# Kernel tuning notes

Hardware: AMD Instinct MI355X
Metric: run time of the kernel (lower is better)

Reference implementation:

```python
import jax, jax.numpy as jnp
import numpy as np
from jax import lax

K = 3
PAD = 1
STRIDE = 1


def setup_inputs() -> dict:
    key = jax.random.key(0)
    k1, k2, k3 = jax.random.split(key, 3)
    B, Cin, Cout, H, W = 4, 64, 64, 128, 128
    x = jax.random.normal(k1, (B, Cin, H, W), dtype=jnp.float32)
    # offset-generating conv weight: [2*K*K, Cin, K, K]
    w_offset = jax.random.normal(k2, (2 * K * K, Cin, K, K), dtype=jnp.float32) * 0.05
    # deformable conv weight: [Cout, Cin, K, K]
    w_deform = jax.random.normal(k3, (Cout, Cin, K, K), dtype=jnp.float32) * 0.05
    return {"x": x, "w_offset": w_offset, "w_deform": w_deform}


def _bilinear_sample_one(img, ys, xs):
    # img: [C, H, W]; ys, xs: [K2, Ho, Wo] float sampling coords
    H, W = img.shape[1], img.shape[2]
    y0 = jnp.floor(ys)
    x0 = jnp.floor(xs)
    wy = ys - y0  # frac weights, [K2, Ho, Wo]
    wx = xs - x0

    def gather(yi, xi):
        valid = (yi >= 0) & (yi <= H - 1) & (xi >= 0) & (xi <= W - 1)
        yc = jnp.clip(yi, 0, H - 1).astype(jnp.int32)
        xc = jnp.clip(xi, 0, W - 1).astype(jnp.int32)
        # img[:, yc, xc] -> [C, K2, Ho, Wo]; zero outside (torchvision zero-pad)
        return img[:, yc, xc] * valid[None].astype(img.dtype)

    v00 = gather(y0, x0)
    v01 = gather(y0, x0 + 1)
    v10 = gather(y0 + 1, x0)
    v11 = gather(y0 + 1, x0 + 1)
    w00 = ((1 - wy) * (1 - wx))[None]
    w01 = ((1 - wy) * wx)[None]
    w10 = (wy * (1 - wx))[None]
    w11 = (wy * wx)[None]
    return v00 * w00 + v01 * w01 + v10 * w10 + v11 * w11  # [C, K2, Ho, Wo]


def reference(x, w_offset, w_deform):
    B, Cin, H, W = x.shape
    Cout = w_deform.shape[0]
    K2 = K * K
    # 1) plain conv to produce offsets: [B, 2*K2, H, W]
    offset = lax.conv_general_dilated(
        x, w_offset, window_strides=(STRIDE, STRIDE),
        padding=((PAD, PAD), (PAD, PAD)),
        dimension_numbers=("NCHW", "OIHW", "NCHW"))
    Ho, Wo = offset.shape[2], offset.shape[3]
    # torchvision ordering: channel 2*k = dy, 2*k+1 = dx, taps row-major
    off = offset.reshape(B, K2, 2, Ho, Wo)
    dy, dx = off[:, :, 0], off[:, :, 1]  # [B, K2, Ho, Wo]
    # 2) base sampling grid per kernel tap
    kk = jnp.arange(K2)
    ki = (kk // K).astype(jnp.float32)  # tap row
    kj = (kk % K).astype(jnp.float32)   # tap col
    base_y = (jnp.arange(Ho, dtype=jnp.float32) * STRIDE - PAD)[None, :] + ki[:, None]  # [K2, Ho]
    base_x = (jnp.arange(Wo, dtype=jnp.float32) * STRIDE - PAD)[None, :] + kj[:, None]  # [K2, Wo]
    ys = base_y[None, :, :, None] + dy  # [B, K2, Ho, Wo]
    xs = base_x[None, :, None, :] + dx
    # 3) deformable bilinear gather: [B, Cin, K2, Ho, Wo]
    sampled = jax.vmap(_bilinear_sample_one)(x, ys, xs)
    # 4) weighted accumulation (the conv contraction)
    out = jnp.einsum("ock,bckhw->bohw", w_deform.reshape(Cout, Cin, K2), sampled)
    return out
```

## Files before the change

kernel.cpp:

```cpp
#include <hip/hip_runtime.h>


#define BATCH 4
#define CIN   64
#define COUT  64
#define HH    128
#define WW    128
#define HWPIX (HH*WW)

typedef __attribute__((ext_vector_type(8))) short short8;
typedef __attribute__((ext_vector_type(4))) float floatx4;

__device__ __forceinline__ unsigned short f2bf(float f) {
  unsigned int u = __float_as_uint(f);
  unsigned int r = u + 0x7fffu + ((u >> 16) & 1u);
  return (unsigned short)(r >> 16);
}
__device__ __forceinline__ float bf2f(unsigned short h) { return __uint_as_float(((unsigned int)h) << 16); }
__device__ __forceinline__ float lo16f(unsigned int u) { return __uint_as_float(u << 16); }
__device__ __forceinline__ float hi16f(unsigned int u) { return __uint_as_float(u & 0xffff0000u); }

__device__ __forceinline__ unsigned int bilin2(unsigned int u00, unsigned int u01,
                                               unsigned int u10, unsigned int u11,
                                               float w00, float w01, float w10, float w11) {
  float lo = w00 * lo16f(u00) + w01 * lo16f(u01) + w10 * lo16f(u10) + w11 * lo16f(u11);
  float hi = w00 * hi16f(u00) + w01 * hi16f(u01) + w10 * hi16f(u10) + w11 * hi16f(u11);
  return (unsigned int)f2bf(lo) | ((unsigned int)f2bf(hi) << 16);
}

__global__ __launch_bounds__(256) void transpose_x_kernel(const float* __restrict__ x,
                                                          unsigned short* __restrict__ xThi,
                                                          unsigned short* __restrict__ xTlo) {
  __shared__ float tile[32][33];
  int b = blockIdx.z, p0 = blockIdx.x * 32, c0 = blockIdx.y * 32;
  int tx = threadIdx.x, ty = threadIdx.y;
  const float* xb = x + (size_t)b * CIN * HWPIX;
  size_t boff = (size_t)b * HWPIX * CIN;
#pragma unroll
  for (int i = 0; i < 4; i++)
    tile[ty + i * 8][tx] = xb[(size_t)(c0 + ty + i * 8) * HWPIX + p0 + tx];
  __syncthreads();
  int wid = ty * 32 + tx;
#pragma unroll
  for (int i = 0; i < 2; i++) {
    int t = wid + i * 256;
    int row = t >> 4;
    int cp = t & 15;
    float v0 = tile[cp * 2][row], v1 = tile[cp * 2 + 1][row];
    unsigned short h0 = f2bf(v0), h1 = f2bf(v1);
    unsigned short l0 = f2bf(v0 - bf2f(h0)), l1 = f2bf(v1 - bf2f(h1));
    size_t o = boff + (size_t)(p0 + row) * CIN + c0 + cp * 2;
    *(ushort2*)&xThi[o] = make_ushort2(h0, h1);
    *(ushort2*)&xTlo[o] = make_ushort2(l0, l1);
  }
}

__global__ __launch_bounds__(256) void prep_weights_kernel(const float* __restrict__ wo,
                                                           const float* __restrict__ wd,
                                                           unsigned short* __restrict__ wdA,
                                                           unsigned short* __restrict__ woAhi,
                                                           unsigned short* __restrict__ woAlo) {
  int t = blockIdx.x * 256 + threadIdx.x;
  if (t < 36864) {
    int j = t & 7, lane = (t >> 3) & 63, ct = (t >> 9) & 3, kc = (t >> 11) & 1, kk = t >> 12;
    int cout = ct * 16 + (lane & 15);
    int cin  = kc * 32 + (lane >> 4) * 8 + j;
    wdA[t] = f2bf(wd[(size_t)(cout * CIN + cin) * 9 + kk]);
  }
  int t2 = t - 36864;
  if (t2 >= 0 && t2 < 18432) {
    int j = t2 & 7, lane = (t2 >> 3) & 63, ct = (t2 >> 9) & 1, kc = (t2 >> 10) & 1, kk = t2 >> 11;
    int cout = ct * 16 + (lane & 15);
    int cin  = kc * 32 + (lane >> 4) * 8 + j;
    float v = (cout < 18) ? wo[(size_t)(cout * CIN + cin) * 9 + kk] : 0.f;
    unsigned short h = f2bf(v);
    woAhi[t2] = h;
    woAlo[t2] = f2bf(v - bf2f(h));
  }
}

__global__ __launch_bounds__(256) void offset_mfma_kernel(const unsigned short* __restrict__ xThi,
                                                          const unsigned short* __restrict__ xTlo,
                                                          const unsigned short* __restrict__ woAhi,
                                                          const unsigned short* __restrict__ woAlo,
                                                          float* __restrict__ offs) {
  __shared__ unsigned short sBhi[4096];
  __shared__ unsigned short sBlo[4096];
  int tid = threadIdx.x;
  int hw = blockIdx.x;
  int bid = (hw & 7) * 128 + (hw >> 3);
  int b = bid >> 8, r = bid & 255, y = r >> 1, x0 = (r & 1) << 6;

  int p1 = tid >> 2, si = tid & 3;
  int lane = tid & 63, w = tid >> 6;

  const unsigned short* xhib = xThi + (size_t)b * HWPIX * CIN;
  const unsigned short* xlob = xTlo + (size_t)b * HWPIX * CIN;

  int wq = p1 >> 4, iq = p1 & 15;
  int kcd = si >> 1, qb = si & 1;
  int dst0 = (((wq * 2 + kcd) * 64) + qb * 32 + iq) * 8;
  int dst1 = dst0 + 128;

  floatx4 acc[2];
  acc[0] = (floatx4){0.f, 0.f, 0.f, 0.f};
  acc[1] = (floatx4){0.f, 0.f, 0.f, 0.f};

  int xp = x0 + p1;

#pragma unroll 1
  for (int kk = 0; kk < 9; kk++) {
    int ys = y - 1 + kk / 3;
    int xs = xp - 1 + kk % 3;
    bool valid = (ys >= 0) && (ys < HH) && (xs >= 0) && (xs < WW);
    uint4 h0 = {0, 0, 0, 0}, h1 = {0, 0, 0, 0}, l0 = {0, 0, 0, 0}, l1 = {0, 0, 0, 0};
    if (valid) {
      const unsigned short* ph = xhib + (size_t)(ys * WW + xs) * CIN + si * 16;
      const unsigned short* pl = xlob + (size_t)(ys * WW + xs) * CIN + si * 16;
      h0 = *(const uint4*)ph; h1 = *(const uint4*)(ph + 8);
      l0 = *(const uint4*)pl; l1 = *(const uint4*)(pl + 8);
    }
    *(uint4*)&sBhi[dst0] = h0; *(uint4*)&sBhi[dst1] = h1;
    *(uint4*)&sBlo[dst0] = l0; *(uint4*)&sBlo[dst1] = l1;
    __syncthreads();
    short8 bh0 = *(const short8*)&sBhi[(w * 2 + 0) * 512 + lane * 8];
    short8 bh1 = *(const short8*)&sBhi[(w * 2 + 1) * 512 + lane * 8];
    short8 bl0 = *(const short8*)&sBlo[(w * 2 + 0) * 512 + lane * 8];
    short8 bl1 = *(const short8*)&sBlo[(w * 2 + 1) * 512 + lane * 8];
    const short8* Ah = (const short8*)(woAhi + (size_t)kk * 2048);
    const short8* Al = (const short8*)(woAlo + (size_t)kk * 2048);
#pragma unroll
    for (int ct = 0; ct < 2; ct++) {
      short8 ah0 = Ah[ct * 64 + lane], ah1 = Ah[128 + ct * 64 + lane];
      short8 al0 = Al[ct * 64 + lane], al1 = Al[128 + ct * 64 + lane];
      acc[ct] = __builtin_amdgcn_mfma_f32_16x16x32_bf16(ah0, bh0, acc[ct], 0, 0, 0);
      acc[ct] = __builtin_amdgcn_mfma_f32_16x16x32_bf16(ah0, bl0, acc[ct], 0, 0, 0);
      acc[ct] = __builtin_amdgcn_mfma_f32_16x16x32_bf16(al0, bh0, acc[ct], 0, 0, 0);
      acc[ct] = __builtin_amdgcn_mfma_f32_16x16x32_bf16(ah1, bh1, acc[ct], 0, 0, 0);
      acc[ct] = __builtin_amdgcn_mfma_f32_16x16x32_bf16(ah1, bl1, acc[ct], 0, 0, 0);
      acc[ct] = __builtin_amdgcn_mfma_f32_16x16x32_bf16(al1, bh1, acc[ct], 0, 0, 0);
    }
    __syncthreads();
  }

  int px = x0 + w * 16 + (lane & 15);
  int rowb = (lane >> 4) * 4;
  float* ob = offs + (size_t)b * 18 * HWPIX + y * WW + px;
#pragma unroll
  for (int ct = 0; ct < 2; ct++)
#pragma unroll
    for (int rr = 0; rr < 4; rr++) {
      int row = ct * 16 + rowb + rr;
      if (row < 18) ob[(size_t)row * HWPIX] = acc[ct][rr];
    }
}

__global__ __launch_bounds__(256) void deform_gemm_kernel(const unsigned short* __restrict__ xT,
                                                          const float* __restrict__ offs,
                                                          const unsigned short* __restrict__ wdA,
                                                          float* __restrict__ out) {
  __shared__ unsigned short sampB[4096];
  int tid = threadIdx.x;
  int hw = blockIdx.x;
  int bid = (hw & 7) * 128 + (hw >> 3);
  int b = bid >> 8, r = bid & 255, y = r >> 1, x0 = (r & 1) << 6;

  int p1 = tid >> 2, si = tid & 3;
  int lane = tid & 63, w = tid >> 6;

  const unsigned short* xTb = xT + (size_t)b * HWPIX * CIN;
  const float* ob = offs + (size_t)b * 18 * HWPIX + y * WW + (x0 + p1);

  int wq = p1 >> 4, iq = p1 & 15;
  int kcd = si >> 1, qb = si & 1;
  int dst0 = (((wq * 2 + kcd) * 64) + qb * 32 + iq) * 8;
  int dst1 = dst0 + 128;

  floatx4 acc[4];
#pragma unroll
  for (int ct = 0; ct < 4; ct++) acc[ct] = (floatx4){0.f, 0.f, 0.f, 0.f};

  int xp = x0 + p1;

#pragma unroll 1
  for (int kk = 0; kk < 9; kk++) {
    {
      float dy = ob[(size_t)(2 * kk) * HWPIX];
      float dx = ob[(size_t)(2 * kk + 1) * HWPIX];
      float ys = (float)(y - 1 + kk / 3) + dy;
      float xs = (float)(xp - 1 + kk % 3) + dx;
      float y0f = floorf(ys), x0f = floorf(xs);
      float wy = ys - y0f, wx = xs - x0f;
      int iy0 = (int)y0f, ix0 = (int)x0f;
      int iy1 = iy0 + 1, ix1 = ix0 + 1;
      float w00 = (1.f - wy) * (1.f - wx), w01 = (1.f - wy) * wx;
      float w10 = wy * (1.f - wx), w11 = wy * wx;
      bool vy0 = (iy0 >= 0) && (iy0 < HH), vy1 = (iy1 >= 0) && (iy1 < HH);
      bool vx0 = (ix0 >= 0) && (ix0 < WW), vx1 = (ix1 >= 0) && (ix1 < WW);
      if (!(vy0 && vx0)) w00 = 0.f;
      if (!(vy0 && vx1)) w01 = 0.f;
      if (!(vy1 && vx0)) w10 = 0.f;
      if (!(vy1 && vx1)) w11 = 0.f;
      int cy0 = min(max(iy0, 0), HH - 1), cy1 = min(max(iy1, 0), HH - 1);
      int cx0 = min(max(ix0, 0), WW - 1), cx1 = min(max(ix1, 0), WW - 1);
      const unsigned short* q00 = xTb + (size_t)(cy0 * WW + cx0) * CIN + si * 16;
      const unsigned short* q01 = xTb + (size_t)(cy0 * WW + cx1) * CIN + si * 16;
      const unsigned short* q10 = xTb + (size_t)(cy1 * WW + cx0) * CIN + si * 16;
      const unsigned short* q11 = xTb + (size_t)(cy1 * WW + cx1) * CIN + si * 16;
      uint4 a00 = *(const uint4*)q00, a01 = *(const uint4*)q01;
      uint4 a10 = *(const uint4*)q10, a11 = *(const uint4*)q11;
      uint4 b00 = *(const uint4*)(q00 + 8), b01 = *(const uint4*)(q01 + 8);
      uint4 b10 = *(const uint4*)(q10 + 8), b11 = *(const uint4*)(q11 + 8);
      uint4 o0, o1;
      o0.x = bilin2(a00.x, a01.x, a10.x, a11.x, w00, w01, w10, w11);
      o0.y = bilin2(a00.y, a01.y, a10.y, a11.y, w00, w01, w10, w11);
      o0.z = bilin2(a00.z, a01.z, a10.z, a11.z, w00, w01, w10, w11);
      o0.w = bilin2(a00.w, a01.w, a10.w, a11.w, w00, w01, w10, w11);
      o1.x = bilin2(b00.x, b01.x, b10.x, b11.x, w00, w01, w10, w11);
      o1.y = bilin2(b00.y, b01.y, b10.y, b11.y, w00, w01, w10, w11);
      o1.z = bilin2(b00.z, b01.z, b10.z, b11.z, w00, w01, w10, w11);
      o1.w = bilin2(b00.w, b01.w, b10.w, b11.w, w00, w01, w10, w11);
      *(uint4*)&sampB[dst0] = o0;
      *(uint4*)&sampB[dst1] = o1;
    }
    __syncthreads();
    {
      short8 bv0 = *(const short8*)&sampB[(w * 2 + 0) * 512 + lane * 8];
      short8 bv1 = *(const short8*)&sampB[(w * 2 + 1) * 512 + lane * 8];
      const short8* Ap = (const short8*)(wdA + (size_t)kk * 4096);
#pragma unroll
      for (int ct = 0; ct < 4; ct++) {
        short8 a0 = Ap[ct * 64 + lane];
        short8 a1 = Ap[256 + ct * 64 + lane];
        acc[ct] = __builtin_amdgcn_mfma_f32_16x16x32_bf16(a0, bv0, acc[ct], 0, 0, 0);
        acc[ct] = __builtin_amdgcn_mfma_f32_16x16x32_bf16(a1, bv1, acc[ct], 0, 0, 0);
      }
    }
    __syncthreads();
  }

  int px = x0 + w * 16 + (lane & 15);
  int rowb = (lane >> 4) * 4;
  float* outb = out + (size_t)b * COUT * HWPIX + y * WW + px;
#pragma unroll
  for (int ct = 0; ct < 4; ct++)
#pragma unroll
    for (int rr = 0; rr < 4; rr++)
      outb[(size_t)(ct * 16 + rowb + rr) * HWPIX] = acc[ct][rr];
}

extern "C" void kernel_launch(void* const* d_in, const int* in_sizes, int n_in,
                              void* d_out, int out_size, void* d_ws, size_t ws_size,
                              hipStream_t stream) {
  const float* x  = (const float*)d_in[0];
  const float* wo = (const float*)d_in[1];
  const float* wd = (const float*)d_in[2];
  float* out = (float*)d_out;

  char* wsb = (char*)d_ws;
  unsigned short* xThi  = (unsigned short*)wsb;
  unsigned short* xTlo  = (unsigned short*)(wsb + 8388608);
  float* offs           = (float*)(wsb + 16777216);
  unsigned short* wdA   = (unsigned short*)(wsb + 16777216 + 4718592);
  unsigned short* woAhi = (unsigned short*)(wsb + 21495808 + 73728);
  unsigned short* woAlo = (unsigned short*)(wsb + 21569536 + 36864);

  transpose_x_kernel<<<dim3(HWPIX / 32, CIN / 32, BATCH), dim3(32, 8, 1), 0, stream>>>(x, xThi, xTlo);
  prep_weights_kernel<<<dim3(216), dim3(256), 0, stream>>>(wo, wd, wdA, woAhi, woAlo);
  offset_mfma_kernel<<<dim3(BATCH * HWPIX / 64), dim3(256), 0, stream>>>(xThi, xTlo, woAhi, woAlo, offs);
  deform_gemm_kernel<<<dim3(BATCH * HWPIX / 64), dim3(256), 0, stream>>>(xThi, offs, wdA, out);
}
```

Baseline: 122.3 us.

## Fuse offset conv into deformable GEMM kernel and merge prep kernels

Merges the x transpose and weight-prep kernels into one launch, and fuses the offset-conv MFMA kernel with the deformable sampling GEMM. Offsets now stay in shared memory per 64-pixel block instead of going through a global buffer, and the sampled tile reuses the sBhi shared buffer. This removes two kernel launches and the global write and read of the offset tensor. The cost is higher per-block shared memory and register pressure in the fused kernel, which may lower occupancy.

After: 114.6 us. 1.07x faster.

```diff
diff --git a/kernel.cpp b/kernel.cpp
--- a/kernel.cpp
+++ b/kernel.cpp
@@ -28,64 +28,70 @@
   return (unsigned int)f2bf(lo) | ((unsigned int)f2bf(hi) << 16);
 }
 
-__global__ __launch_bounds__(256) void transpose_x_kernel(const float* __restrict__ x,
-                                                          unsigned short* __restrict__ xThi,
-                                                          unsigned short* __restrict__ xTlo) {
-  __shared__ float tile[32][33];
-  int b = blockIdx.z, p0 = blockIdx.x * 32, c0 = blockIdx.y * 32;
-  int tx = threadIdx.x, ty = threadIdx.y;
-  const float* xb = x + (size_t)b * CIN * HWPIX;
-  size_t boff = (size_t)b * HWPIX * CIN;
-#pragma unroll
-  for (int i = 0; i < 4; i++)
-    tile[ty + i * 8][tx] = xb[(size_t)(c0 + ty + i * 8) * HWPIX + p0 + tx];
-  __syncthreads();
-  int wid = ty * 32 + tx;
-#pragma unroll
-  for (int i = 0; i < 2; i++) {
-    int t = wid + i * 256;
-    int row = t >> 4;
-    int cp = t & 15;
-    float v0 = tile[cp * 2][row], v1 = tile[cp * 2 + 1][row];
-    unsigned short h0 = f2bf(v0), h1 = f2bf(v1);
-    unsigned short l0 = f2bf(v0 - bf2f(h0)), l1 = f2bf(v1 - bf2f(h1));
-    size_t o = boff + (size_t)(p0 + row) * CIN + c0 + cp * 2;
-    *(ushort2*)&xThi[o] = make_ushort2(h0, h1);
-    *(ushort2*)&xTlo[o] = make_ushort2(l0, l1);
-  }
-}
-
-__global__ __launch_bounds__(256) void prep_weights_kernel(const float* __restrict__ wo,
-                                                           const float* __restrict__ wd,
-                                                           unsigned short* __restrict__ wdA,
-                                                           unsigned short* __restrict__ woAhi,
-                                                           unsigned short* __restrict__ woAlo) {
-  int t = blockIdx.x * 256 + threadIdx.x;
-  if (t < 36864) {
-    int j = t & 7, lane = (t >> 3) & 63, ct = (t >> 9) & 3, kc = (t >> 11) & 1, kk = t >> 12;
-    int cout = ct * 16 + (lane & 15);
-    int cin  = kc * 32 + (lane >> 4) * 8 + j;
-    wdA[t] = f2bf(wd[(size_t)(cout * CIN + cin) * 9 + kk]);
-  }
-  int t2 = t - 36864;
-  if (t2 >= 0 && t2 < 18432) {
-    int j = t2 & 7, lane = (t2 >> 3) & 63, ct = (t2 >> 9) & 1, kc = (t2 >> 10) & 1, kk = t2 >> 11;
-    int cout = ct * 16 + (lane & 15);
-    int cin  = kc * 32 + (lane >> 4) * 8 + j;
-    float v = (cout < 18) ? wo[(size_t)(cout * CIN + cin) * 9 + kk] : 0.f;
-    unsigned short h = f2bf(v);
-    woAhi[t2] = h;
-    woAlo[t2] = f2bf(v - bf2f(h));
-  }
-}
-
-__global__ __launch_bounds__(256) void offset_mfma_kernel(const unsigned short* __restrict__ xThi,
-                                                          const unsigned short* __restrict__ xTlo,
-                                                          const unsigned short* __restrict__ woAhi,
-                                                          const unsigned short* __restrict__ woAlo,
-                                                          float* __restrict__ offs) {
+__global__ __launch_bounds__(256) void pre_kernel(const float* __restrict__ x,
+                                                  const float* __restrict__ wo,
+                                                  const float* __restrict__ wd,
+                                                  unsigned short* __restrict__ xThi,
+                                                  unsigned short* __restrict__ xTlo,
+                                                  unsigned short* __restrict__ wdA,
+                                                  unsigned short* __restrict__ woAhi,
+                                                  unsigned short* __restrict__ woAlo) {
+  int tid = threadIdx.x;
+  if (blockIdx.x < 4096) {
+    __shared__ float tile[32][33];
+    int t = blockIdx.x;
+    int b = t >> 10, rem = t & 1023;
+    int c0 = (rem >> 9) * 32, p0 = (rem & 511) * 32;
+    int tx = tid & 31, ty = tid >> 5;
+    const float* xb = x + (size_t)b * CIN * HWPIX;
+    size_t boff = (size_t)b * HWPIX * CIN;
+#pragma unroll
+    for (int i = 0; i < 4; i++)
+      tile[ty + i * 8][tx] = xb[(size_t)(c0 + ty + i * 8) * HWPIX + p0 + tx];
+    __syncthreads();
+#pragma unroll
+    for (int i = 0; i < 2; i++) {
+      int tt = tid + i * 256;
+      int row = tt >> 4;
+      int cp = tt & 15;
+      float v0 = tile[cp * 2][row], v1 = tile[cp * 2 + 1][row];
+      unsigned short h0 = f2bf(v0), h1 = f2bf(v1);
+      unsigned short l0 = f2bf(v0 - bf2f(h0)), l1 = f2bf(v1 - bf2f(h1));
+      size_t o = boff + (size_t)(p0 + row) * CIN + c0 + cp * 2;
+      *(ushort2*)&xThi[o] = make_ushort2(h0, h1);
+      *(ushort2*)&xTlo[o] = make_ushort2(l0, l1);
+    }
+  } else {
+    int t = (blockIdx.x - 4096) * 256 + tid;
+    if (t < 36864) {
+      int j = t & 7, lane = (t >> 3) & 63, ct = (t >> 9) & 3, kc = (t >> 11) & 1, kk = t >> 12;
+      int cout = ct * 16 + (lane & 15);
+      int cin  = kc * 32 + (lane >> 4) * 8 + j;
+      wdA[t] = f2bf(wd[(size_t)(cout * CIN + cin) * 9 + kk]);
+    }
+    int t2 = t - 36864;
+    if (t2 >= 0 && t2 < 18432) {
+      int j = t2 & 7, lane = (t2 >> 3) & 63, ct = (t2 >> 9) & 1, kc = (t2 >> 10) & 1, kk = t2 >> 11;
+      int cout = ct * 16 + (lane & 15);
+      int cin  = kc * 32 + (lane >> 4) * 8 + j;
+      float v = (cout < 18) ? wo[(size_t)(cout * CIN + cin) * 9 + kk] : 0.f;
+      unsigned short h = f2bf(v);
+      woAhi[t2] = h;
+      woAlo[t2] = f2bf(v - bf2f(h));
+    }
+  }
+}
+
+__global__ __launch_bounds__(256) void fused_dcn_kernel(const unsigned short* __restrict__ xThi,
+                                                        const unsigned short* __restrict__ xTlo,
+                                                        const unsigned short* __restrict__ woAhi,
+                                                        const unsigned short* __restrict__ woAlo,
+                                                        const unsigned short* __restrict__ wdA,
+                                                        float* __restrict__ out) {
   __shared__ unsigned short sBhi[4096];
   __shared__ unsigned short sBlo[4096];
+  __shared__ float offL[18 * 64];
+
   int tid = threadIdx.x;
   int hw = blockIdx.x;
   int bid = (hw & 7) * 128 + (hw >> 3);
@@ -101,12 +107,11 @@
   int kcd = si >> 1, qb = si & 1;
   int dst0 = (((wq * 2 + kcd) * 64) + qb * 32 + iq) * 8;
   int dst1 = dst0 + 128;
-
-  floatx4 acc[2];
-  acc[0] = (floatx4){0.f, 0.f, 0.f, 0.f};
-  acc[1] = (floatx4){0.f, 0.f, 0.f, 0.f};
-
   int xp = x0 + p1;
+
+  floatx4 oacc[2];
+  oacc[0] = (floatx4){0.f, 0.f, 0.f, 0.f};
+  oacc[1] = (floatx4){0.f, 0.f, 0.f, 0.f};
 
 #pragma unroll 1
   for (int kk = 0; kk < 9; kk++) {
@@ -133,60 +138,38 @@
     for (int ct = 0; ct < 2; ct++) {
       short8 ah0 = Ah[ct * 64 + lane], ah1 = Ah[128 + ct * 64 + lane];
       short8 al0 = Al[ct * 64 + lane], al1 = Al[128 + ct * 64 + lane];
-      acc[ct] = __builtin_amdgcn_mfma_f32_16x16x32_bf16(ah0, bh0, acc[ct], 0, 0, 0);
-      acc[ct] = __builtin_amdgcn_mfma_f32_16x16x32_bf16(ah0, bl0, acc[ct], 0, 0, 0);
-      acc[ct] = __builtin_amdgcn_mfma_f32_16x16x32_bf16(al0, bh0, acc[ct], 0, 0, 0);
-      acc[ct] = __builtin_amdgcn_mfma_f32_16x16x32_bf16(ah1, bh1, acc[ct], 0, 0, 0);
-      acc[ct] = __builtin_amdgcn_mfma_f32_16x16x32_bf16(ah1, bl1, acc[ct], 0, 0, 0);
-      acc[ct] = __builtin_amdgcn_mfma_f32_16x16x32_bf16(al1, bh1, acc[ct], 0, 0, 0);
-    }
-    __syncthreads();
-  }
-
-  int px = x0 + w * 16 + (lane & 15);
-  int rowb = (lane >> 4) * 4;
-  float* ob = offs + (size_t)b * 18 * HWPIX + y * WW + px;
-#pragma unroll
-  for (int ct = 0; ct < 2; ct++)
-#pragma unroll
-    for (int rr = 0; rr < 4; rr++) {
-      int row = ct * 16 + rowb + rr;
-      if (row < 18) ob[(size_t)row * HWPIX] = acc[ct][rr];
-    }
-}
-
-__global__ __launch_bounds__(256) void deform_gemm_kernel(const unsigned short* __restrict__ xT,
-                                                          const float* __restrict__ offs,
-                                                          const unsigned short* __restrict__ wdA,
-                                                          float* __restrict__ out) {
-  __shared__ unsigned short sampB[4096];
-  int tid = threadIdx.x;
-  int hw = blockIdx.x;
-  int bid = (hw & 7) * 128 + (hw >> 3);
-  int b = bid >> 8, r = bid & 255, y = r >> 1, x0 = (r & 1) << 6;
-
-  int p1 = tid >> 2, si = tid & 3;
-  int lane = tid & 63, w = tid >> 6;
-
-  const unsigned short* xTb = xT + (size_t)b * HWPIX * CIN;
-  const float* ob = offs + (size_t)b * 18 * HWPIX + y * WW + (x0 + p1);
-
-  int wq = p1 >> 4, iq = p1 & 15;
-  int kcd = si >> 1, qb = si & 1;
-  int dst0 = (((wq * 2 + kcd) * 64) + qb * 32 + iq) * 8;
-  int dst1 = dst0 + 128;
+      oacc[ct] = __builtin_amdgcn_mfma_f32_16x16x32_bf16(ah0, bh0, oacc[ct], 0, 0, 0);
+      oacc[ct] = __builtin_amdgcn_mfma_f32_16x16x32_bf16(ah0, bl0, oacc[ct], 0, 0, 0);
+      oacc[ct] = __builtin_amdgcn_mfma_f32_16x16x32_bf16(al0, bh0, oacc[ct], 0, 0, 0);
+      oacc[ct] = __builtin_amdgcn_mfma_f32_16x16x32_bf16(ah1, bh1, oacc[ct], 0, 0, 0);
+      oacc[ct] = __builtin_amdgcn_mfma_f32_16x16x32_bf16(ah1, bl1, oacc[ct], 0, 0, 0);
+      oacc[ct] = __builtin_amdgcn_mfma_f32_16x16x32_bf16(al1, bh1, oacc[ct], 0, 0, 0);
+    }
+    __syncthreads();
+  }
+
+  {
+    int pxl = w * 16 + (lane & 15);
+    int rowb = (lane >> 4) * 4;
+#pragma unroll
+    for (int ct = 0; ct < 2; ct++)
+#pragma unroll
+      for (int rr = 0; rr < 4; rr++) {
+        int row = ct * 16 + rowb + rr;
+        if (row < 18) offL[row * 64 + pxl] = oacc[ct][rr];
+      }
+  }
+  __syncthreads();
 
   floatx4 acc[4];
 #pragma unroll
   for (int ct = 0; ct < 4; ct++) acc[ct] = (floatx4){0.f, 0.f, 0.f, 0.f};
-
-  int xp = x0 + p1;
 
 #pragma unroll 1
   for (int kk = 0; kk < 9; kk++) {
     {
-      float dy = ob[(size_t)(2 * kk) * HWPIX];
-      float dx = ob[(size_t)(2 * kk + 1) * HWPIX];
+      float dy = offL[(2 * kk) * 64 + p1];
+      float dx = offL[(2 * kk + 1) * 64 + p1];
       float ys = (float)(y - 1 + kk / 3) + dy;
       float xs = (float)(xp - 1 + kk % 3) + dx;
       float y0f = floorf(ys), x0f = floorf(xs);
@@ -203,10 +186,10 @@
       if (!(vy1 && vx1)) w11 = 0.f;
       int cy0 = min(max(iy0, 0), HH - 1), cy1 = min(max(iy1, 0), HH - 1);
       int cx0 = min(max(ix0, 0), WW - 1), cx1 = min(max(ix1, 0), WW - 1);
-      const unsigned short* q00 = xTb + (size_t)(cy0 * WW + cx0) * CIN + si * 16;
-      const unsigned short* q01 = xTb + (size_t)(cy0 * WW + cx1) * CIN + si * 16;
-      const unsigned short* q10 = xTb + (size_t)(cy1 * WW + cx0) * CIN + si * 16;
-      const unsigned short* q11 = xTb + (size_t)(cy1 * WW + cx1) * CIN + si * 16;
+      const unsigned short* q00 = xhib + (size_t)(cy0 * WW + cx0) * CIN + si * 16;
+      const unsigned short* q01 = xhib + (size_t)(cy0 * WW + cx1) * CIN + si * 16;
+      const unsigned short* q10 = xhib + (size_t)(cy1 * WW + cx0) * CIN + si * 16;
+      const unsigned short* q11 = xhib + (size_t)(cy1 * WW + cx1) * CIN + si * 16;
       uint4 a00 = *(const uint4*)q00, a01 = *(const uint4*)q01;
       uint4 a10 = *(const uint4*)q10, a11 = *(const uint4*)q11;
       uint4 b00 = *(const uint4*)(q00 + 8), b01 = *(const uint4*)(q01 + 8);
@@ -220,13 +203,13 @@
       o1.y = bilin2(b00.y, b01.y, b10.y, b11.y, w00, w01, w10, w11);
       o1.z = bilin2(b00.z, b01.z, b10.z, b11.z, w00, w01, w10, w11);
       o1.w = bilin2(b00.w, b01.w, b10.w, b11.w, w00, w01, w10, w11);
-      *(uint4*)&sampB[dst0] = o0;
-      *(uint4*)&sampB[dst1] = o1;
+      *(uint4*)&sBhi[dst0] = o0;
+      *(uint4*)&sBhi[dst1] = o1;
     }
     __syncthreads();
     {
-      short8 bv0 = *(const short8*)&sampB[(w * 2 + 0) * 512 + lane * 8];
-      short8 bv1 = *(const short8*)&sampB[(w * 2 + 1) * 512 + lane * 8];
+      short8 bv0 = *(const short8*)&sBhi[(w * 2 + 0) * 512 + lane * 8];
+      short8 bv1 = *(const short8*)&sBhi[(w * 2 + 1) * 512 + lane * 8];
       const short8* Ap = (const short8*)(wdA + (size_t)kk * 4096);
 #pragma unroll
       for (int ct = 0; ct < 4; ct++) {
@@ -260,13 +243,10 @@
   char* wsb = (char*)d_ws;
   unsigned short* xThi  = (unsigned short*)wsb;
   unsigned short* xTlo  = (unsigned short*)(wsb + 8388608);
-  float* offs           = (float*)(wsb + 16777216);
-  unsigned short* wdA   = (unsigned short*)(wsb + 16777216 + 4718592);
-  unsigned short* woAhi = (unsigned short*)(wsb + 21495808 + 73728);
-  unsigned short* woAlo = (unsigned short*)(wsb + 21569536 + 36864);
-
-  transpose_x_kernel<<<dim3(HWPIX / 32, CIN / 32, BATCH), dim3(32, 8, 1), 0, stream>>>(x, xThi, xTlo);
-  prep_weights_kernel<<<dim3(216), dim3(256), 0, stream>>>(wo, wd, wdA, woAhi, woAlo);
-  offset_mfma_kernel<<<dim3(BATCH * HWPIX / 64), dim3(256), 0, stream>>>(xThi, xTlo, woAhi, woAlo, offs);
-  deform_gemm_kernel<<<dim3(BATCH * HWPIX / 64), dim3(256), 0, stream>>>(xThi, offs, wdA, out);
-}
+  unsigned short* wdA   = (unsigned short*)(wsb + 16777216);
+  unsigned short* woAhi = (unsigned short*)(wsb + 16777216 + 73728);
+  unsigned short* woAlo = (unsigned short*)(wsb + 16850944 + 36864);
+
+  pre_kernel<<<dim3(4096 + 216), dim3(256), 0, stream>>>(x, wo, wd, xThi, xTlo, wdA, woAhi, woAlo);
+  fused_dcn_kernel<<<dim3(BATCH * HWPIX / 64), dim3(256), 0, stream>>>(xThi, xTlo, woAhi, woAlo, wdA, out);
+}
```
